# Kernel optimization log

Measured on AMD Instinct MI355X. Metric: run time of the kernel, lower is better.

## Reference

```python
import jax, jax.numpy as jnp
import numpy as np
import math

N_HEAD = 16
N_KV_HEAD = 4
N_EMBED = 2048
HEAD_DIM = N_EMBED // N_HEAD  # 128
ROPE_BASE = 10000.0


def _rope_tables(T, dim, dtype):
    inv_freq = 1.0 / (ROPE_BASE ** (jnp.arange(0, dim, 2, dtype=jnp.float32) / dim))
    t = jnp.arange(T, dtype=jnp.float32)
    freqs = jnp.outer(t, inv_freq)            # (T, dim/2)
    emb = jnp.concatenate([freqs, freqs], -1) # (T, dim)
    return jnp.cos(emb).astype(dtype), jnp.sin(emb).astype(dtype)


def _rotate_half(x):
    half = x.shape[-1] // 2
    return jnp.concatenate([-x[..., half:], x[..., :half]], axis=-1)


def setup_inputs() -> dict:
    key = jax.random.key(0)
    kx, kq, kk, kv, ko = jax.random.split(key, 5)
    B, T, C = 2, 2048, N_EMBED
    s = 0.02
    return {
        "x": jax.random.normal(kx, (B, T, C), jnp.float32),
        "Wq": jax.random.normal(kq, (N_HEAD * HEAD_DIM, C), jnp.float32) * s,
        "Wk": jax.random.normal(kk, (N_KV_HEAD * HEAD_DIM, C), jnp.float32) * s,
        "Wv": jax.random.normal(kv, (N_KV_HEAD * HEAD_DIM, C), jnp.float32) * s,
        "Wo": jax.random.normal(ko, (C, N_HEAD * HEAD_DIM), jnp.float32) * s,
    }


def reference(x, Wq, Wk, Wv, Wo):
    B, T, C = x.shape
    H, KV, D = N_HEAD, N_KV_HEAD, HEAD_DIM
    rep = H // KV

    q = jnp.einsum('btc,oc->bto', x, Wq).reshape(B, T, H, D).transpose(0, 2, 1, 3)   # (B,H,T,D)
    k = jnp.einsum('btc,oc->bto', x, Wk).reshape(B, T, KV, D).transpose(0, 2, 1, 3)  # (B,KV,T,D)
    v = jnp.einsum('btc,oc->bto', x, Wv).reshape(B, T, KV, D).transpose(0, 2, 1, 3)

    cos, sin = _rope_tables(T, D, x.dtype)  # (T,D) broadcast over (B,h,T,D)
    q = q * cos + _rotate_half(q) * sin
    k = k * cos + _rotate_half(k) * sin

    # GQA: head h attends to kv head h // rep (== repeat_interleave in torch).
    qg = q.reshape(B, KV, rep, T, D)
    scale = 1.0 / math.sqrt(D)
    attn = jnp.einsum('bgrtd,bgsd->bgrts', qg, k) * scale  # (B,KV,rep,T,T)
    causal = jnp.tril(jnp.ones((T, T), dtype=bool))
    attn = jnp.where(causal, attn, -jnp.inf)
    attn = jax.nn.softmax(attn, axis=-1)
    out = jnp.einsum('bgrts,bgsd->bgrtd', attn, v)          # (B,KV,rep,T,D)
    out = out.reshape(B, H, T, D).transpose(0, 2, 1, 3).reshape(B, T, H * D)
    return jnp.einsum('bto,co->btc', out, Wo)
```

## Files before the change

### kernel.cpp

```cpp
#include <hip/hip_runtime.h>
#include <stdint.h>

typedef unsigned short u16;
typedef __attribute__((ext_vector_type(8))) short short8;
typedef __attribute__((ext_vector_type(4))) short short4v;
typedef __attribute__((ext_vector_type(4))) float f32x4;

#define NB_  2
#define NT_  2048
#define NC_  2048
#define NH_  16
#define NKV_ 4
#define HD_  128
#define NM_  (NB_*NT_)

__device__ __forceinline__ u16 f2b(float x) {
  uint32_t u = __float_as_uint(x);
  u += 0x7fffu + ((u >> 16) & 1u);
  return (u16)(u >> 16);
}
__device__ __forceinline__ float b2f(u16 x) {
  return __uint_as_float(((uint32_t)x) << 16);
}
__device__ __forceinline__ uint32_t pk2(float a, float b) {
  return (uint32_t)f2b(a) | ((uint32_t)f2b(b) << 16);
}

typedef __attribute__((address_space(1))) uint32_t* gp1_t;
typedef __attribute__((address_space(3))) uint32_t* lp3_t;
__device__ __forceinline__ void async_ld16(const void* g, void* l) {
  __builtin_amdgcn_global_load_lds((gp1_t)(uintptr_t)g, (lp3_t)(uintptr_t)l, 16, 0, 0);
}

__global__ void f2bf_all(const float* __restrict__ x,  const float* __restrict__ wq,
                         const float* __restrict__ wk, const float* __restrict__ wv,
                         const float* __restrict__ wo,
                         u16* xb, u16* wqb, u16* wkb, u16* wvb, u16* wob) {
  int bid = blockIdx.x;
  const float* src; u16* dst; int base;
  if      (bid < 8192)  { src = x;  dst = xb;  base = bid; }
  else if (bid < 12288) { src = wq; dst = wqb; base = bid - 8192; }
  else if (bid < 13312) { src = wk; dst = wkb; base = bid - 12288; }
  else if (bid < 14336) { src = wv; dst = wvb; base = bid - 13312; }
  else                  { src = wo; dst = wob; base = bid - 14336; }
  int i = base * 256 + threadIdx.x;
  const float4 v = ((const float4*)src)[i];
  short4v o;
  o[0] = (short)f2b(v.x); o[1] = (short)f2b(v.y);
  o[2] = (short)f2b(v.z); o[3] = (short)f2b(v.w);
  *(short4v*)(dst + (size_t)i * 4) = o;
}

__global__ void postk(const u16* __restrict__ qraw, const u16* __restrict__ kraw,
                      const u16* __restrict__ vraw,
                      u16* __restrict__ Qr, u16* __restrict__ Kr, u16* __restrict__ Vt) {
  __shared__ u16 tile[64][72];
  int bid = blockIdx.x;
  if (bid < 20480) {
    const u16* raw; u16* out; int nheads; int tid; float osc;
    if (bid < 16384) { raw = qraw; out = Qr; nheads = NH_;  tid = bid * 256 + threadIdx.x;
                       osc = 0.08838834764831845f; }
    else             { raw = kraw; out = Kr; nheads = NKV_; tid = (bid - 16384) * 256 + threadIdx.x;
                       osc = 1.0f; }
    int j = tid & 63;
    int t = (tid >> 6) & (NT_ - 1);
    int bh = tid >> 17;
    int h = bh % nheads, b = bh / nheads;
    const u16* src = raw + ((size_t)(b * NT_ + t) * nheads + h) * HD_;
    float q0 = b2f(src[j]), q1 = b2f(src[j + 64]);
    float inv = expf(-0.14391156831212787f * (float)j);
    float ang = (float)t * inv;
    float c = cosf(ang), s = sinf(ang);
    u16* dst = out + ((size_t)(b * nheads + h) * NT_ + t) * HD_;
    dst[j]      = f2b((q0 * c - q1 * s) * osc);
    dst[j + 64] = f2b((q1 * c + q0 * s) * osc);
  } else {
    int idx = bid - 20480;
    int tt = idx & 63, dd = idx >> 6;
    int tid = threadIdx.x;
    int r = tid >> 3, c8 = (tid & 7) * 8;
#pragma unroll
    for (int it = 0; it < 2; ++it) {
      int row = r + it * 32;
      short8 v = *(const short8*)(vraw + (size_t)(tt * 64 + row) * (NKV_ * HD_) + dd * 64 + c8);
      *(short8*)(&tile[row][c8]) = v;
    }
    __syncthreads();
    int b = (tt * 64) >> 11, t0 = (tt * 64) & (NT_ - 1);
    int dl = tid >> 3, t8 = (tid & 7) * 8;
#pragma unroll
    for (int it = 0; it < 2; ++it) {
      int d = dl + it * 32;
      int gcol = dd * 64 + d;
      int kv = gcol >> 7, drow = gcol & 127;
      short8 v;
#pragma unroll
      for (int k = 0; k < 8; ++k) v[k] = (short)tile[t8 + k][d];
      *(short8*)(Vt + ((size_t)(b * NKV_ + kv) * HD_ + drow) * NT_ + t0 + t8) = v;
    }
  }
}

template<int FOUT>
__global__ __launch_bounds__(256, 3)
void gemm128(const u16* __restrict__ A,
             const u16* __restrict__ B1, void* __restrict__ C1, int N1,
             const u16* __restrict__ B2, void* __restrict__ C2, int N2,
             const u16* __restrict__ B3, void* __restrict__ C3, int N3,
             int s1, int s2, int K)
{
  __shared__ u16 As[2 * 128 * 32];
  __shared__ u16 Bs[2 * 128 * 32];
  int bx = blockIdx.x;
  const int by = blockIdx.y;
  const u16* Bmat; void* Cmat; int N;
  if      (bx < s1) { Bmat = B1; Cmat = C1; N = N1; }
  else if (bx < s2) { Bmat = B2; Cmat = C2; N = N2; bx -= s1; }
  else              { Bmat = B3; Cmat = C3; N = N3; bx -= s2; }
  const int m0 = by * 128, n0 = bx * 128;
  const int tid = threadIdx.x;
  const int wave = tid >> 6, lane = tid & 63;
  const int quad = lane >> 4, l15 = lane & 15;
  const int wm = wave >> 1, wn = wave & 1;

  const int p_local = lane >> 3;
  const int s7 = lane & 7;
  const int mlo = s7 >> 2;
  const int gg = (s7 & 3) ^ (p_local & 3);
  const int rowc = p_local * 2 + mlo;
  const int kel = gg * 8;

  const u16* Ag[2]; const u16* Bg[2];
  u16* Al[2]; u16* Bl[2];
#pragma unroll
  for (int q = 0; q < 2; ++q) {
    const int c = wave * 2 + q;
    Ag[q] = A    + (size_t)(m0 + c * 16 + rowc) * K + kel;
    Bg[q] = Bmat + (size_t)(n0 + c * 16 + rowc) * K + kel;
    Al[q] = As + c * 512;
    Bl[q] = Bs + c * 512;
  }

  f32x4 acc[4][4] = {};

  int a_addr[4], b_addr[4];
#pragma unroll
  for (int i = 0; i < 4; ++i) {
    int m = wm * 64 + i * 16 + l15;
    a_addr[i] = ((m >> 1) * 8 + (m & 1) * 4 + (quad ^ ((m >> 1) & 3))) * 8;
    int n = wn * 64 + i * 16 + l15;
    b_addr[i] = ((n >> 1) * 8 + (n & 1) * 4 + (quad ^ ((n >> 1) & 3))) * 8;
  }

  const int nk = K >> 5;
#pragma unroll
  for (int q = 0; q < 2; ++q) {
    async_ld16(Ag[q], Al[q]);
    async_ld16(Bg[q], Bl[q]);
  }

  for (int i = 0; i < nk; ++i) {
    __syncthreads();
    if (i + 1 < nk) {
      const int off = ((i + 1) & 1) * 4096;
      const int k0 = (i + 1) << 5;
#pragma unroll
      for (int q = 0; q < 2; ++q) {
        async_ld16(Ag[q] + k0, Al[q] + off);
        async_ld16(Bg[q] + k0, Bl[q] + off);
      }
    }
    const int off = (i & 1) * 4096;
    short8 af[4], bf[4];
#pragma unroll
    for (int j = 0; j < 4; ++j) af[j] = *(const short8*)(As + off + a_addr[j]);
#pragma unroll
    for (int j = 0; j < 4; ++j) bf[j] = *(const short8*)(Bs + off + b_addr[j]);
#pragma unroll
    for (int mb = 0; mb < 4; ++mb)
#pragma unroll
      for (int nb = 0; nb < 4; ++nb)
        acc[mb][nb] = __builtin_amdgcn_mfma_f32_16x16x32_bf16(af[mb], bf[nb], acc[mb][nb], 0, 0, 0);
  }

#pragma unroll
  for (int mb = 0; mb < 4; ++mb)
#pragma unroll
    for (int nb = 0; nb < 4; ++nb) {
      const int gn = n0 + wn * 64 + nb * 16 + l15;
#pragma unroll
      for (int r = 0; r < 4; ++r) {
        const int gm = m0 + wm * 64 + mb * 16 + quad * 4 + r;
        const float v = acc[mb][nb][r];
        if (FOUT) ((float*)Cmat)[(size_t)gm * N + gn] = v;
        else      ((u16*)Cmat)[(size_t)gm * N + gn] = f2b(v);
      }
    }
}

__global__ __launch_bounds__(256, 2)
void attn_kernel(const u16* __restrict__ Q, const u16* __restrict__ Kg,
                 const u16* __restrict__ Vt, u16* __restrict__ O)
{
  __shared__ u16 Ks[2 * 8192];
  __shared__ u16 Vs[2 * 8192];
  const int bx = blockIdx.x;
  const int h  = blockIdx.y;
  const int b  = blockIdx.z;
  const int qi = b ? (15 - bx) : bx;
  const int kv = h >> 2;
  const int tid = threadIdx.x;
  const int wave = tid >> 6, lane = tid & 63;
  const int quad = lane >> 4, l15 = lane & 15;
  const int qw = qi * 128 + wave * 32;

  const u16* Kbase = Kg + (size_t)(b * NKV_ + kv) * NT_ * HD_;
  const u16* Vbase = Vt + (size_t)(b * NKV_ + kv) * HD_ * NT_;

  short8 qf[2][4];
#pragma unroll
  for (int qs = 0; qs < 2; ++qs) {
    const u16* qb = Q + ((size_t)(b * NH_ + h) * NT_ + qw + qs * 16 + l15) * HD_ + quad * 8;
#pragma unroll
    for (int kb = 0; kb < 4; ++kb) qf[qs][kb] = *(const short8*)(qb + kb * 32);
  }

  const int krow = lane >> 4, kgs = lane & 15;
  const int vrow = lane >> 3, vgs = lane & 7;

  auto stage = [&](int kt, int pbuf) {
    u16* KsB = Ks + pbuf * 8192;
    u16* VsB = Vs + pbuf * 8192;
#pragma unroll
    for (int qq = 0; qq < 4; ++qq) {
      const int c = wave * 4 + qq;
      const int rk = c * 4 + krow;
      const int gk = kgs ^ (rk & 7);
      async_ld16(Kbase + (size_t)(kt * 64 + rk) * HD_ + gk * 8, KsB + c * 512);
      const int rv = c * 8 + vrow;
      const int gv = vgs ^ (rv & 7);
      async_ld16(Vbase + (size_t)rv * NT_ + kt * 64 + gv * 8, VsB + c * 512);
    }
  };

  f32x4 acc_o[2][8] = {};
  float l_st[2] = {0.f, 0.f};
  const int nkt = 2 * qi + 2;

  stage(0, 0);

  for (int kt = 0; kt < nkt; ++kt) {
    __syncthreads();
    if (kt + 1 < nkt) stage(kt + 1, (kt + 1) & 1);
    if (kt * 64 > qw + 31) continue;

    const u16* KsB = Ks + (kt & 1) * 8192;
    const u16* VsB = Vs + (kt & 1) * 8192;

    f32x4 S[2][4] = {};
#pragma unroll
    for (int nb = 0; nb < 4; ++nb) {
      const int row = nb * 16 + l15;
#pragma unroll
      for (int kb = 0; kb < 4; ++kb) {
        const int gi = kb * 4 + quad;
        short8 kfr = *(const short8*)(KsB + row * 128 + (gi ^ (row & 7)) * 8);
        S[0][nb] = __builtin_amdgcn_mfma_f32_16x16x32_bf16(kfr, qf[0][kb], S[0][nb], 0, 0, 0);
        S[1][nb] = __builtin_amdgcn_mfma_f32_16x16x32_bf16(kfr, qf[1][kb], S[1][nb], 0, 0, 0);
      }
    }

#pragma unroll
    for (int qs = 0; qs < 2; ++qs) {
      if (kt * 64 + 63 > qw + qs * 16) {
        const int qg = qw + qs * 16 + l15;
#pragma unroll
        for (int nb = 0; nb < 4; ++nb)
#pragma unroll
          for (int r = 0; r < 4; ++r) {
            const int key = kt * 64 + nb * 16 + quad * 4 + r;
            if (key > qg) S[qs][nb][r] = -INFINITY;
          }
      }
    }

#pragma unroll
    for (int qs = 0; qs < 2; ++qs) {
      float rs = 0.f;
#pragma unroll
      for (int nb = 0; nb < 4; ++nb)
#pragma unroll
        for (int r = 0; r < 4; ++r) {
          const float p = __expf(S[qs][nb][r]);
          S[qs][nb][r] = p;
          rs += p;
        }
      rs += __shfl_xor(rs, 16);
      rs += __shfl_xor(rs, 32);
      l_st[qs] += rs;
    }

    short8 pf[2][2];
#pragma unroll
    for (int qs = 0; qs < 2; ++qs) {
      uint32_t d0[4], d1[4];
#pragma unroll
      for (int nb = 0; nb < 4; ++nb) {
        d0[nb] = pk2(S[qs][nb][0], S[qs][nb][1]);
        d1[nb] = pk2(S[qs][nb][2], S[qs][nb][3]);
      }
      const int srcA = ((quad & 1) * 2) * 16 + l15;
      const int srcB = srcA + 16;
      const bool hi = quad >= 2;
#pragma unroll
      for (int k2 = 0; k2 < 2; ++k2) {
        const int nbL = k2 * 2, nbH = k2 * 2 + 1;
        uint32_t a0 = (uint32_t)__shfl((int)d0[nbL], srcA);
        uint32_t a1 = (uint32_t)__shfl((int)d1[nbL], srcA);
        uint32_t a2 = (uint32_t)__shfl((int)d0[nbL], srcB);
        uint32_t a3 = (uint32_t)__shfl((int)d1[nbL], srcB);
        uint32_t b0 = (uint32_t)__shfl((int)d0[nbH], srcA);
        uint32_t b1 = (uint32_t)__shfl((int)d1[nbH], srcA);
        uint32_t b2 = (uint32_t)__shfl((int)d0[nbH], srcB);
        uint32_t b3 = (uint32_t)__shfl((int)d1[nbH], srcB);
        uint32_t w[4] = { hi ? b0 : a0, hi ? b1 : a1, hi ? b2 : a2, hi ? b3 : a3 };
        pf[qs][k2] = *(short8*)w;
      }
    }

#pragma unroll
    for (int db = 0; db < 8; ++db) {
      const int row = db * 16 + l15;
#pragma unroll
      for (int k2 = 0; k2 < 2; ++k2) {
        const int gi = k2 * 4 + quad;
        short8 vf = *(const short8*)(VsB + row * 64 + (gi ^ (row & 7)) * 8);
        acc_o[0][db] = __builtin_amdgcn_mfma_f32_16x16x32_bf16(pf[0][k2], vf, acc_o[0][db], 0, 0, 0);
        acc_o[1][db] = __builtin_amdgcn_mfma_f32_16x16x32_bf16(pf[1][k2], vf, acc_o[1][db], 0, 0, 0);
      }
    }
  }

#pragma unroll
  for (int qs = 0; qs < 2; ++qs) {
    const float linv = 1.f / l_st[qs];
    float inv_r[4];
#pragma unroll
    for (int r = 0; r < 4; ++r) inv_r[r] = __shfl(linv, quad * 4 + r);
    const size_t orow = ((size_t)b * NT_ + qw + qs * 16) * (NH_ * HD_);
#pragma unroll
    for (int db = 0; db < 8; ++db)
#pragma unroll
      for (int r = 0; r < 4; ++r)
        O[orow + (size_t)(quad * 4 + r) * (NH_ * HD_) + h * HD_ + db * 16 + l15] =
            f2b(acc_o[qs][db][r] * inv_r[r]);
  }
}

extern "C" void kernel_launch(void* const* d_in, const int* in_sizes, int n_in,
                              void* d_out, int out_size, void* d_ws, size_t ws_size,
                              hipStream_t stream) {
  const float* x  = (const float*)d_in[0];
  const float* Wq = (const float*)d_in[1];
  const float* Wk = (const float*)d_in[2];
  const float* Wv = (const float*)d_in[3];
  const float* Wo = (const float*)d_in[4];
  float* out = (float*)d_out;
  char* ws = (char*)d_ws;
  const size_t MB = (size_t)1 << 20;
  u16* xb   = (u16*)(ws + 0);
  u16* wqb  = (u16*)(ws + 16 * MB);
  u16* wkb  = (u16*)(ws + 24 * MB);
  u16* wvb  = (u16*)(ws + 26 * MB);
  u16* wob  = (u16*)(ws + 28 * MB);
  u16* qraw = (u16*)(ws + 36 * MB);
  u16* kraw = (u16*)(ws + 52 * MB);
  u16* vraw = (u16*)(ws + 56 * MB);
  u16* Qr   = (u16*)(ws + 60 * MB);
  u16* Kr   = (u16*)(ws + 76 * MB);
  u16* Vtb  = (u16*)(ws + 80 * MB);
  u16* Ob   = xb;

  f2bf_all<<<18432, 256, 0, stream>>>(x, Wq, Wk, Wv, Wo, xb, wqb, wkb, wvb, wob);

  gemm128<0><<<dim3(24, 32), 256, 0, stream>>>(xb, wqb, qraw, 2048,
                                               wkb, kraw, 512,
                                               wvb, vraw, 512, 16, 20, 2048);

  postk<<<20992, 256, 0, stream>>>(qraw, kraw, vraw, Qr, Kr, Vtb);

  attn_kernel<<<dim3(16, 16, 2), 256, 0, stream>>>(Qr, Kr, Vtb, Ob);

  gemm128<1><<<dim3(16, 32), 256, 0, stream>>>(Ob, wob, out, 2048,
                                               wob, out, 2048,
                                               wob, out, 2048, 16, 32, 2048);
}
```

Measured before the change: 307.7 us.

## Fuse QKV projection into 192-wide GEMM and compute softmax row sums via MFMA

The Q, K and V projections now run as one GEMM with 128x192 tiles over a fused contiguous weight buffer. This cuts the grid from 768 to 512 blocks and writes a single interleaved QKV output that the RoPE/transpose kernel reads directly. In attention, the per-row softmax sum is computed with extra MFMAs against a ones vector instead of scalar adds and cross-lane shuffles. P is packed to bf16 by truncation rather than rounding. The fused weights rely on wq, wk and wv being laid out contiguously in the workspace. Truncation slightly changes numerics, and the larger GEMM tile raises register pressure, so occupancy drops to 2 blocks per CU.

```diff
diff --git a/kernel.cpp b/kernel.cpp
--- a/kernel.cpp
+++ b/kernel.cpp
@@ -13,6 +13,7 @@
 #define NKV_ 4
 #define HD_  128
 #define NM_  (NB_*NT_)
+#define NQKV 3072
 
 __device__ __forceinline__ u16 f2b(float x) {
   uint32_t u = __float_as_uint(x);
@@ -22,8 +23,8 @@
 __device__ __forceinline__ float b2f(u16 x) {
   return __uint_as_float(((uint32_t)x) << 16);
 }
-__device__ __forceinline__ uint32_t pk2(float a, float b) {
-  return (uint32_t)f2b(a) | ((uint32_t)f2b(b) << 16);
+__device__ __forceinline__ uint32_t pk2t(float a, float b) {
+  return (__float_as_uint(a) >> 16) | (__float_as_uint(b) & 0xFFFF0000u);
 }
 
 typedef __attribute__((address_space(1))) uint32_t* gp1_t;
@@ -51,22 +52,21 @@
   *(short4v*)(dst + (size_t)i * 4) = o;
 }
 
-__global__ void postk(const u16* __restrict__ qraw, const u16* __restrict__ kraw,
-                      const u16* __restrict__ vraw,
+__global__ void postk(const u16* __restrict__ qkv,
                       u16* __restrict__ Qr, u16* __restrict__ Kr, u16* __restrict__ Vt) {
   __shared__ u16 tile[64][72];
   int bid = blockIdx.x;
   if (bid < 20480) {
-    const u16* raw; u16* out; int nheads; int tid; float osc;
-    if (bid < 16384) { raw = qraw; out = Qr; nheads = NH_;  tid = bid * 256 + threadIdx.x;
+    u16* out; int nheads; int tid; int coff; float osc;
+    if (bid < 16384) { out = Qr; nheads = NH_;  tid = bid * 256 + threadIdx.x; coff = 0;
                        osc = 0.08838834764831845f; }
-    else             { raw = kraw; out = Kr; nheads = NKV_; tid = (bid - 16384) * 256 + threadIdx.x;
+    else             { out = Kr; nheads = NKV_; tid = (bid - 16384) * 256 + threadIdx.x; coff = 2048;
                        osc = 1.0f; }
     int j = tid & 63;
     int t = (tid >> 6) & (NT_ - 1);
     int bh = tid >> 17;
     int h = bh % nheads, b = bh / nheads;
-    const u16* src = raw + ((size_t)(b * NT_ + t) * nheads + h) * HD_;
+    const u16* src = qkv + ((size_t)(b * NT_ + t)) * NQKV + coff + h * HD_;
     float q0 = b2f(src[j]), q1 = b2f(src[j + 64]);
     float inv = expf(-0.14391156831212787f * (float)j);
     float ang = (float)t * inv;
@@ -82,7 +82,7 @@
 #pragma unroll
     for (int it = 0; it < 2; ++it) {
       int row = r + it * 32;
-      short8 v = *(const short8*)(vraw + (size_t)(tt * 64 + row) * (NKV_ * HD_) + dd * 64 + c8);
+      short8 v = *(const short8*)(qkv + (size_t)(tt * 64 + row) * NQKV + 2560 + dd * 64 + c8);
       *(short8*)(&tile[row][c8]) = v;
     }
     __syncthreads();
@@ -101,23 +101,13 @@
   }
 }
 
-template<int FOUT>
-__global__ __launch_bounds__(256, 3)
-void gemm128(const u16* __restrict__ A,
-             const u16* __restrict__ B1, void* __restrict__ C1, int N1,
-             const u16* __restrict__ B2, void* __restrict__ C2, int N2,
-             const u16* __restrict__ B3, void* __restrict__ C3, int N3,
-             int s1, int s2, int K)
+__global__ __launch_bounds__(256, 2)
+void gemm192(const u16* __restrict__ A, const u16* __restrict__ B, u16* __restrict__ C, int K)
 {
   __shared__ u16 As[2 * 128 * 32];
-  __shared__ u16 Bs[2 * 128 * 32];
-  int bx = blockIdx.x;
-  const int by = blockIdx.y;
-  const u16* Bmat; void* Cmat; int N;
-  if      (bx < s1) { Bmat = B1; Cmat = C1; N = N1; }
-  else if (bx < s2) { Bmat = B2; Cmat = C2; N = N2; bx -= s1; }
-  else              { Bmat = B3; Cmat = C3; N = N3; bx -= s2; }
-  const int m0 = by * 128, n0 = bx * 128;
+  __shared__ u16 Bs[2 * 192 * 32];
+  const int bx = blockIdx.x, by = blockIdx.y;
+  const int m0 = by * 128, n0 = bx * 192;
   const int tid = threadIdx.x;
   const int wave = tid >> 6, lane = tid & 63;
   const int quad = lane >> 4, l15 = lane & 15;
@@ -130,13 +120,105 @@
   const int rowc = p_local * 2 + mlo;
   const int kel = gg * 8;
 
+  const u16* Ag[2]; u16* Al[2];
+#pragma unroll
+  for (int q = 0; q < 2; ++q) {
+    const int c = wave * 2 + q;
+    Ag[q] = A + (size_t)(m0 + c * 16 + rowc) * K + kel;
+    Al[q] = As + c * 512;
+  }
+  const u16* Bg[3]; u16* Bl[3];
+#pragma unroll
+  for (int q = 0; q < 3; ++q) {
+    const int c = wave * 3 + q;
+    Bg[q] = B + (size_t)(n0 + c * 16 + rowc) * K + kel;
+    Bl[q] = Bs + c * 512;
+  }
+
+  f32x4 acc[4][6] = {};
+
+  int a_addr[4], b_addr[6];
+#pragma unroll
+  for (int i = 0; i < 4; ++i) {
+    int m = wm * 64 + i * 16 + l15;
+    a_addr[i] = ((m >> 1) * 8 + (m & 1) * 4 + (quad ^ ((m >> 1) & 3))) * 8;
+  }
+#pragma unroll
+  for (int i = 0; i < 6; ++i) {
+    int n = wn * 96 + i * 16 + l15;
+    b_addr[i] = ((n >> 1) * 8 + (n & 1) * 4 + (quad ^ ((n >> 1) & 3))) * 8;
+  }
+
+  const int nk = K >> 5;
+#pragma unroll
+  for (int q = 0; q < 2; ++q) async_ld16(Ag[q], Al[q]);
+#pragma unroll
+  for (int q = 0; q < 3; ++q) async_ld16(Bg[q], Bl[q]);
+
+  for (int i = 0; i < nk; ++i) {
+    __syncthreads();
+    if (i + 1 < nk) {
+      const int offA = ((i + 1) & 1) * 4096;
+      const int offB = ((i + 1) & 1) * 6144;
+      const int k0 = (i + 1) << 5;
+#pragma unroll
+      for (int q = 0; q < 2; ++q) async_ld16(Ag[q] + k0, Al[q] + offA);
+#pragma unroll
+      for (int q = 0; q < 3; ++q) async_ld16(Bg[q] + k0, Bl[q] + offB);
+    }
+    const int offA = (i & 1) * 4096;
+    const int offB = (i & 1) * 6144;
+    short8 af[4], bf[6];
+#pragma unroll
+    for (int j = 0; j < 4; ++j) af[j] = *(const short8*)(As + offA + a_addr[j]);
+#pragma unroll
+    for (int j = 0; j < 6; ++j) bf[j] = *(const short8*)(Bs + offB + b_addr[j]);
+#pragma unroll
+    for (int mb = 0; mb < 4; ++mb)
+#pragma unroll
+      for (int nb = 0; nb < 6; ++nb)
+        acc[mb][nb] = __builtin_amdgcn_mfma_f32_16x16x32_bf16(af[mb], bf[nb], acc[mb][nb], 0, 0, 0);
+  }
+
+#pragma unroll
+  for (int mb = 0; mb < 4; ++mb)
+#pragma unroll
+    for (int nb = 0; nb < 6; ++nb) {
+      const int gn = n0 + wn * 96 + nb * 16 + l15;
+#pragma unroll
+      for (int r = 0; r < 4; ++r) {
+        const int gm = m0 + wm * 64 + mb * 16 + quad * 4 + r;
+        C[(size_t)gm * NQKV + gn] = f2b(acc[mb][nb][r]);
+      }
+    }
+}
+
+__global__ __launch_bounds__(256, 2)
+void gemm128o(const u16* __restrict__ A, const u16* __restrict__ B, float* __restrict__ C, int K)
+{
+  __shared__ u16 As[2 * 128 * 32];
+  __shared__ u16 Bs[2 * 128 * 32];
+  const int bx = blockIdx.x, by = blockIdx.y;
+  const int m0 = by * 128, n0 = bx * 128;
+  const int tid = threadIdx.x;
+  const int wave = tid >> 6, lane = tid & 63;
+  const int quad = lane >> 4, l15 = lane & 15;
+  const int wm = wave >> 1, wn = wave & 1;
+
+  const int p_local = lane >> 3;
+  const int s7 = lane & 7;
+  const int mlo = s7 >> 2;
+  const int gg = (s7 & 3) ^ (p_local & 3);
+  const int rowc = p_local * 2 + mlo;
+  const int kel = gg * 8;
+
   const u16* Ag[2]; const u16* Bg[2];
   u16* Al[2]; u16* Bl[2];
 #pragma unroll
   for (int q = 0; q < 2; ++q) {
     const int c = wave * 2 + q;
-    Ag[q] = A    + (size_t)(m0 + c * 16 + rowc) * K + kel;
-    Bg[q] = Bmat + (size_t)(n0 + c * 16 + rowc) * K + kel;
+    Ag[q] = A + (size_t)(m0 + c * 16 + rowc) * K + kel;
+    Bg[q] = B + (size_t)(n0 + c * 16 + rowc) * K + kel;
     Al[q] = As + c * 512;
     Bl[q] = Bs + c * 512;
   }
@@ -191,9 +273,7 @@
 #pragma unroll
       for (int r = 0; r < 4; ++r) {
         const int gm = m0 + wm * 64 + mb * 16 + quad * 4 + r;
-        const float v = acc[mb][nb][r];
-        if (FOUT) ((float*)Cmat)[(size_t)gm * N + gn] = v;
-        else      ((u16*)Cmat)[(size_t)gm * N + gn] = f2b(v);
+        C[(size_t)gm * NC_ + gn] = acc[mb][nb][r];
       }
     }
 }
@@ -243,8 +323,12 @@
     }
   };
 
+  short8 vone;
+#pragma unroll
+  for (int j = 0; j < 8; ++j) vone[j] = (short)0x3F80;
+
   f32x4 acc_o[2][8] = {};
-  float l_st[2] = {0.f, 0.f};
+  f32x4 acc_l[2] = {};
   const int nkt = 2 * qi + 2;
 
   stage(0, 0);
@@ -285,20 +369,12 @@
     }
 
 #pragma unroll
-    for (int qs = 0; qs < 2; ++qs) {
-      float rs = 0.f;
+    for (int qs = 0; qs < 2; ++qs)
 #pragma unroll
       for (int nb = 0; nb < 4; ++nb)
 #pragma unroll
-        for (int r = 0; r < 4; ++r) {
-          const float p = __expf(S[qs][nb][r]);
-          S[qs][nb][r] = p;
-          rs += p;
-        }
-      rs += __shfl_xor(rs, 16);
-      rs += __shfl_xor(rs, 32);
-      l_st[qs] += rs;
-    }
+        for (int r = 0; r < 4; ++r)
+          S[qs][nb][r] = __expf(S[qs][nb][r]);
 
     short8 pf[2][2];
 #pragma unroll
@@ -306,8 +382,8 @@
       uint32_t d0[4], d1[4];
 #pragma unroll
       for (int nb = 0; nb < 4; ++nb) {
-        d0[nb] = pk2(S[qs][nb][0], S[qs][nb][1]);
-        d1[nb] = pk2(S[qs][nb][2], S[qs][nb][3]);
+        d0[nb] = pk2t(S[qs][nb][0], S[qs][nb][1]);
+        d1[nb] = pk2t(S[qs][nb][2], S[qs][nb][3]);
       }
       const int srcA = ((quad & 1) * 2) * 16 + l15;
       const int srcB = srcA + 16;
@@ -329,6 +405,12 @@
     }
 
 #pragma unroll
+    for (int qs = 0; qs < 2; ++qs) {
+      acc_l[qs] = __builtin_amdgcn_mfma_f32_16x16x32_bf16(pf[qs][0], vone, acc_l[qs], 0, 0, 0);
+      acc_l[qs] = __builtin_amdgcn_mfma_f32_16x16x32_bf16(pf[qs][1], vone, acc_l[qs], 0, 0, 0);
+    }
+
+#pragma unroll
     for (int db = 0; db < 8; ++db) {
       const int row = db * 16 + l15;
 #pragma unroll
@@ -343,10 +425,9 @@
 
 #pragma unroll
   for (int qs = 0; qs < 2; ++qs) {
-    const float linv = 1.f / l_st[qs];
     float inv_r[4];
 #pragma unroll
-    for (int r = 0; r < 4; ++r) inv_r[r] = __shfl(linv, quad * 4 + r);
+    for (int r = 0; r < 4; ++r) inv_r[r] = 1.f / acc_l[qs][r];
     const size_t orow = ((size_t)b * NT_ + qw + qs * 16) * (NH_ * HD_);
 #pragma unroll
     for (int db = 0; db < 8; ++db)
@@ -368,30 +449,24 @@
   float* out = (float*)d_out;
   char* ws = (char*)d_ws;
   const size_t MB = (size_t)1 << 20;
-  u16* xb   = (u16*)(ws + 0);
-  u16* wqb  = (u16*)(ws + 16 * MB);
-  u16* wkb  = (u16*)(ws + 24 * MB);
-  u16* wvb  = (u16*)(ws + 26 * MB);
-  u16* wob  = (u16*)(ws + 28 * MB);
-  u16* qraw = (u16*)(ws + 36 * MB);
-  u16* kraw = (u16*)(ws + 52 * MB);
-  u16* vraw = (u16*)(ws + 56 * MB);
-  u16* Qr   = (u16*)(ws + 60 * MB);
-  u16* Kr   = (u16*)(ws + 76 * MB);
-  u16* Vtb  = (u16*)(ws + 80 * MB);
-  u16* Ob   = xb;
-
-  f2bf_all<<<18432, 256, 0, stream>>>(x, Wq, Wk, Wv, Wo, xb, wqb, wkb, wvb, wob);
-
-  gemm128<0><<<dim3(24, 32), 256, 0, stream>>>(xb, wqb, qraw, 2048,
-                                               wkb, kraw, 512,
-                                               wvb, vraw, 512, 16, 20, 2048);
-
-  postk<<<20992, 256, 0, stream>>>(qraw, kraw, vraw, Qr, Kr, Vtb);
+  u16* xb    = (u16*)(ws + 0);
+  u16* wqkv  = (u16*)(ws + 16 * MB);
+  u16* wkb   = (u16*)(ws + 24 * MB);
+  u16* wvb   = (u16*)(ws + 26 * MB);
+  u16* wob   = (u16*)(ws + 28 * MB);
+  u16* qkvrw = (u16*)(ws + 36 * MB);
+  u16* Qr    = (u16*)(ws + 60 * MB);
+  u16* Kr    = (u16*)(ws + 76 * MB);
+  u16* Vtb   = (u16*)(ws + 80 * MB);
+  u16* Ob    = xb;
+
+  f2bf_all<<<18432, 256, 0, stream>>>(x, Wq, Wk, Wv, Wo, xb, wqkv, wkb, wvb, wob);
+
+  gemm192<<<dim3(16, 32), 256, 0, stream>>>(xb, wqkv, qkvrw, 2048);
+
+  postk<<<20992, 256, 0, stream>>>(qkvrw, Qr, Kr, Vtb);
 
   attn_kernel<<<dim3(16, 16, 2), 256, 0, stream>>>(Qr, Kr, Vtb, Ob);
 
-  gemm128<1><<<dim3(16, 32), 256, 0, stream>>>(Ob, wob, out, 2048,
-                                               wob, out, 2048,
-                                               wob, out, 2048, 16, 32, 2048);
-}
+  gemm128o<<<dim3(16, 32), 256, 0, stream>>>(Ob, wob, out, 2048);
+}
```

Measured after the change: 287.5 us. -6.5%, faster.
